# Kernel tuning notes

Hardware: AMD Instinct MI355X
Metric: run time of the kernel (lower is better)

Reference implementation:

```python
import jax, jax.numpy as jnp
import numpy as np
from jax.scipy.special import logsumexp

N, K, D = 131072, 256, 32


def setup_inputs() -> dict:
    key = jax.random.key(0)
    k1, k2, k3 = jax.random.split(key, 3)
    points = jax.random.normal(k1, (N, D), dtype=jnp.float32)
    centers = jax.random.uniform(k2, (K, D), dtype=jnp.float32)
    # well-conditioned inverse-sqrt covariances (original used 15*I; scaled to
    # avoid float32 overflow in sqrt(det(covs_inv)) for D=32)
    covs_inv_sqrt = (0.5 * jnp.broadcast_to(jnp.eye(D, dtype=jnp.float32), (K, D, D))
                     + 0.02 * jax.random.normal(k3, (K, D, D), dtype=jnp.float32))
    weights = jnp.ones((K,), dtype=jnp.float32)
    threshold = jnp.zeros((1,), dtype=jnp.float32)
    return {"points": points, "centers": centers,
            "covs_inv_sqrt": covs_inv_sqrt, "weights": weights,
            "threshold": threshold}


def reference(points, centers, covs_inv_sqrt, weights, threshold):
    # refresh(): equal_clusters=True branch
    w = jnp.abs(weights)
    center_prs = w / (w.sum() + 1e-30)                       # [K]
    covs_inv = jnp.einsum('kde,kfe->kdf', covs_inv_sqrt, covs_inv_sqrt)  # [K,D,D]
    coefs = center_prs * jnp.sqrt(jnp.linalg.det(covs_inv))  # [K]

    # pairwise weighted sqdist: q_ij = (x_i - c_j)^T A_j (x_i - c_j)
    B = covs_inv.reshape(K, D * D)                           # [K, D*D]
    X2 = (points[:, :, None] * points[:, None, :]).reshape(N, D * D)  # [N, D*D]
    t_xAx = X2 @ B.T                                         # [N, K]
    m = jnp.einsum('kde,ke->kd', covs_inv, centers)          # A_j c_j, [K,D]
    t_xAc = points @ m.T                                     # [N, K]
    t_cAc = jnp.einsum('kd,kd->k', m, centers)               # [K]
    d_ij = -0.5 * (t_xAx - 2.0 * t_xAc + t_cAc[None, :])     # [N, K]

    # weighted logsumexp over centers, then subtract threshold
    ll = logsumexp(d_ij, axis=1, b=coefs[None, :])           # [N]
    return ll[:, None] - threshold[0]                        # [N, 1]
```

## Files before the change

### kernel.cpp

```cpp
#include <hip/hip_runtime.h>
#include <math.h>

#define NPTS 131072
#define KCOMP 256
#define DIM 32
#define NREAL 560
#define NCH 18
#define PSIF_BYTES 294912
#define WS_NEED (PSIF_BYTES + KCOMP * 4)

typedef __attribute__((ext_vector_type(8))) short short8;
typedef __attribute__((ext_vector_type(16))) float f32x16;

__device__ __forceinline__ unsigned short f2bf(float v) {
    unsigned u = __float_as_uint(v);
    u += 0x7fffu + ((u >> 16) & 1u);
    return (unsigned short)(u >> 16);
}

__device__ __forceinline__ unsigned pkbf(float lo, float hi) {
#if __has_builtin(__builtin_amdgcn_perm)
    const unsigned a = __float_as_uint(hi) + 0x8000u;
    const unsigned b = __float_as_uint(lo) + 0x8000u;
    return __builtin_amdgcn_perm(a, b, 0x07060302u);
#else
    return (unsigned)f2bf(lo) | ((unsigned)f2bf(hi) << 16);
#endif
}

__device__ __forceinline__ void dma16(const uint4* g, uint4* s) {
    __builtin_amdgcn_global_load_lds(
        (const __attribute__((address_space(1))) void*)g,
        (__attribute__((address_space(3))) void*)s, 16, 0, 0);
}

constexpr int PfxT(int d) { return 32 * d - (d * (d - 1)) / 2; }
constexpr int rowT(int p) { int d = 0; while (d < 31 && PfxT(d + 1) <= p) ++d; return d; }
constexpr int colT(int p) { return rowT(p) + (p - PfxT(rowT(p))); }

template<int P, int J>
__device__ __forceinline__ float genOne(const float (&x)[DIM]) {
    constexpr int p = P + J;
    if constexpr (p >= NREAL) {
        return 0.f;
    } else if constexpr (p >= 528) {
        return x[p - 528];
    } else {
        constexpr int d = rowT(p);
        constexpr int f = colT(p);
        static_assert(d >= 0 && d < 32 && f >= d && f < 32, "bad feature map");
        return x[d] * x[f];
    }
}

__global__ __launch_bounds__(256) void gmm_pre(
    const float* __restrict__ S,
    const float* __restrict__ centers,
    const float* __restrict__ weights,
    unsigned short* __restrict__ PsiF,
    float* __restrict__ kc2)
{
    __shared__ float Sl[DIM][DIM + 1];
    __shared__ float As[DIM][DIM + 1];
    __shared__ float cl[DIM], ml[DIM];
    __shared__ float red[256];

    const int k = blockIdx.x, tid = threadIdx.x;

    for (int idx = tid; idx < DIM * DIM; idx += 256)
        Sl[idx >> 5][idx & 31] = S[(size_t)k * DIM * DIM + idx];
    if (tid < DIM) cl[tid] = centers[k * DIM + tid];
    __syncthreads();

    for (int idx = tid; idx < DIM * DIM; idx += 256) {
        const int d = idx >> 5, f = idx & 31;
        float a = 0.f;
#pragma unroll
        for (int e = 0; e < DIM; ++e) a = fmaf(Sl[d][e], Sl[f][e], a);
        As[d][f] = a;
    }
    __syncthreads();

    if (tid < DIM) {
        float mv = 0.f;
#pragma unroll
        for (int f = 0; f < DIM; ++f) mv = fmaf(As[tid][f], cl[f], mv);
        ml[tid] = mv;
    }
    __syncthreads();

    for (int p = tid; p < NREAL; p += 256) {
        float val;
        if (p < 528) {
            int d = 0, pr = 0;
            while (pr + (32 - d) <= p) { pr += (32 - d); ++d; }
            const int f = d + (p - pr);
            val = (f == d) ? -0.5f * As[d][d] : -As[d][f];
        } else {
            val = ml[p - 528];
        }
        const int c = p >> 6, kk = p & 63;
        const int s = kk >> 4, qq = (kk >> 3) & 1, j = kk & 7;
        const int ct = k >> 5, ll = qq * 32 + (k & 31);
        const int g = c * 2048 + (s * 8 + ct) * 64 + ll;
        PsiF[(size_t)g * 8 + j] = f2bf(val);
    }

    red[tid] = fabsf(weights[tid]);
    __syncthreads();
    for (int off = 128; off > 0; off >>= 1) {
        if (tid < off) red[tid] += red[tid + off];
        __syncthreads();
    }
    const float wsum = red[0];

    for (int j = 0; j < DIM - 1; ++j) {
        const float inv = 1.0f / As[j][j];
        for (int idx = tid; idx < DIM * DIM; idx += 256) {
            const int r = idx >> 5, c = idx & 31;
            if (r > j && c > j)
                As[r][c] = fmaf(-As[r][j] * inv, As[j][c], As[r][c]);
        }
        __syncthreads();
    }

    if (tid < DIM) red[tid] = __logf(As[tid][tid]);
    __syncthreads();
    if (tid == 0) {
        float sl = 0.f;
        for (int j = 0; j < DIM; ++j) sl += red[j];
        float cac = 0.f;
        for (int d2 = 0; d2 < DIM; ++d2) cac = fmaf(ml[d2], cl[d2], cac);
        kc2[k] = __logf(fabsf(weights[k])) - __logf(wsum + 1e-30f)
               + 0.5f * sl - 0.5f * cac;
    }
}

template<int P>
__device__ __forceinline__ void genQuad(const float (&x)[DIM], float* v) {
    v[0] = genOne<P, 0>(x);
    v[1] = genOne<P, 1>(x);
    v[2] = genOne<P, 2>(x);
    v[3] = genOne<P, 3>(x);
}

template<int CH, int SS>
__device__ __forceinline__ void genSite(const float (&x)[DIM], uint4* base,
                                        int rbg, int r32) {
    float v[8];
    genQuad<CH * 32 + SS * 8>(x, v);
    genQuad<CH * 32 + SS * 8 + 4>(x, v + 4);
    uint4 u;
    u.x = pkbf(v[0], v[1]);
    u.y = pkbf(v[2], v[3]);
    u.z = pkbf(v[4], v[5]);
    u.w = pkbf(v[6], v[7]);
    base[(SS >> 1) * 256 + rbg * 64 + (SS & 1) * 32 + r32] = u;
}

template<int CH>
__device__ __forceinline__ void genChunk(const float (&x)[DIM], uint4* sA4,
                                         int q, int rbg, int r32) {
    uint4* base = sA4 + (CH & 1) * 512;
    if constexpr (CH < 17) {
        if (q == 0)      genSite<CH, 0>(x, base, rbg, r32);
        else if (q == 1) genSite<CH, 1>(x, base, rbg, r32);
        else if (q == 2) genSite<CH, 2>(x, base, rbg, r32);
        else             genSite<CH, 3>(x, base, rbg, r32);
    } else {
        if (q == 0)      genSite<CH, 0>(x, base, rbg, r32);
        else if (q == 1) genSite<CH, 1>(x, base, rbg, r32);
    }
}

template<int C>
__device__ __forceinline__ void doChunk(const float (&x)[DIM],
    uint4* sA4, uint4* sB4, const uint4* __restrict__ PsiF4,
    f32x16 (&acc)[4],
    int l, int w, int q, int rbg, int r32, int rb, int c0)
{

    if constexpr (C + 1 < NCH) {
        constexpr int NI = (C + 1 == 17) ? 1 : 2;
        const uint4* src = PsiF4 + (C + 1) * 1024 + w * 64 + l;
        uint4* dst = sB4 + ((C + 1) & 1) * 1024 + w * 64 + l;
#pragma unroll
        for (int i = 0; i < NI; ++i) dma16(src + i * 512, dst + i * 512);
    }

    if constexpr (C + 1 < NCH) genChunk<C + 1>(x, sA4, q, rbg, r32);

    constexpr int NS = (C < 17) ? 2 : 1;
    const uint4* aa = sA4 + (C & 1) * 512;
    const uint4* bb = sB4 + (C & 1) * 1024;
#pragma unroll
    for (int s = 0; s < NS; ++s) {
        short8 a = __builtin_bit_cast(short8, aa[(s * 4 + rb) * 64 + l]);
#pragma unroll
        for (int j = 0; j < 4; ++j) {
            short8 b = __builtin_bit_cast(short8, bb[(s * 8 + c0 + j) * 64 + l]);
            acc[j] = __builtin_amdgcn_mfma_f32_32x32x16_bf16(a, b, acc[j], 0, 0, 0);
        }
    }

    __syncthreads();
}

__device__ __forceinline__ void epiHalf(const f32x16 (&acc)[4], const float (&kcv)[4],
    int rblock, int l, int whalf, float (*sM)[2], float (*sS)[2])
{
#pragma unroll
    for (int rg = 0; rg < 16; ++rg) {
        float vals[4], m = -INFINITY;
#pragma unroll
        for (int j = 0; j < 4; ++j) { vals[j] = acc[j][rg] + kcv[j]; m = fmaxf(m, vals[j]); }
#pragma unroll
        for (int mask = 1; mask < 32; mask <<= 1) m = fmaxf(m, __shfl_xor(m, mask, 64));
        float sv = 0.f;
#pragma unroll
        for (int j = 0; j < 4; ++j) sv += __expf(vals[j] - m);
#pragma unroll
        for (int mask = 1; mask < 32; mask <<= 1) sv += __shfl_xor(sv, mask, 64);
        if ((l & 31) == 0) {
            const int R = rblock * 32 + (rg & 3) + 8 * (rg >> 2) + 4 * (l >> 5);
            sM[R][whalf] = m; sS[R][whalf] = sv;
        }
    }
}

__global__ __launch_bounds__(512, 4) void gmm_mfma(
    const float* __restrict__ points,
    const unsigned short* __restrict__ PsiF,
    const float* __restrict__ kc2,
    const float* __restrict__ thr,
    float* __restrict__ out)
{
    __shared__ uint4 sA4[1024];
    __shared__ uint4 sB4[2048];
    float (*sM)[2] = (float (*)[2])sA4;
    float (*sS)[2] = (float (*)[2])(sA4 + 64);

    const int t = threadIdx.x;
    const int w = t >> 6, l = t & 63;
    const int row = t & 127, q = t >> 7;
    const int rbg = row >> 5, r32 = row & 31;
    const int rb = w >> 1, c0 = (w & 1) * 4;

    const uint4* PsiF4 = (const uint4*)PsiF;

    {
        const uint4* src = PsiF4 + w * 64 + l;
        uint4* dst = sB4 + w * 64 + l;
        dma16(src, dst);
        dma16(src + 512, dst + 512);
    }

    float x[DIM];
    const float4* px = (const float4*)(points + ((size_t)blockIdx.x * 128 + row) * DIM);
#pragma unroll
    for (int j2 = 0; j2 < 8; ++j2) {
        float4 v = px[j2];
        x[4 * j2 + 0] = v.x; x[4 * j2 + 1] = v.y;
        x[4 * j2 + 2] = v.z; x[4 * j2 + 3] = v.w;
    }

    f32x16 acc[4];
#pragma unroll
    for (int j = 0; j < 4; ++j)
#pragma unroll
        for (int r = 0; r < 16; ++r) acc[j][r] = 0.f;

    genChunk<0>(x, sA4, q, rbg, r32);
    __syncthreads();

    doChunk<0>(x, sA4, sB4, PsiF4, acc, l, w, q, rbg, r32, rb, c0);
    doChunk<1>(x, sA4, sB4, PsiF4, acc, l, w, q, rbg, r32, rb, c0);
    doChunk<2>(x, sA4, sB4, PsiF4, acc, l, w, q, rbg, r32, rb, c0);
    doChunk<3>(x, sA4, sB4, PsiF4, acc, l, w, q, rbg, r32, rb, c0);
    doChunk<4>(x, sA4, sB4, PsiF4, acc, l, w, q, rbg, r32, rb, c0);
    doChunk<5>(x, sA4, sB4, PsiF4, acc, l, w, q, rbg, r32, rb, c0);
    doChunk<6>(x, sA4, sB4, PsiF4, acc, l, w, q, rbg, r32, rb, c0);
    doChunk<7>(x, sA4, sB4, PsiF4, acc, l, w, q, rbg, r32, rb, c0);
    doChunk<8>(x, sA4, sB4, PsiF4, acc, l, w, q, rbg, r32, rb, c0);
    doChunk<9>(x, sA4, sB4, PsiF4, acc, l, w, q, rbg, r32, rb, c0);
    doChunk<10>(x, sA4, sB4, PsiF4, acc, l, w, q, rbg, r32, rb, c0);
    doChunk<11>(x, sA4, sB4, PsiF4, acc, l, w, q, rbg, r32, rb, c0);
    doChunk<12>(x, sA4, sB4, PsiF4, acc, l, w, q, rbg, r32, rb, c0);
    doChunk<13>(x, sA4, sB4, PsiF4, acc, l, w, q, rbg, r32, rb, c0);
    doChunk<14>(x, sA4, sB4, PsiF4, acc, l, w, q, rbg, r32, rb, c0);
    doChunk<15>(x, sA4, sB4, PsiF4, acc, l, w, q, rbg, r32, rb, c0);
    doChunk<16>(x, sA4, sB4, PsiF4, acc, l, w, q, rbg, r32, rb, c0);
    doChunk<17>(x, sA4, sB4, PsiF4, acc, l, w, q, rbg, r32, rb, c0);

    float kcv[4];
#pragma unroll
    for (int j = 0; j < 4; ++j) kcv[j] = kc2[(c0 + j) * 32 + (l & 31)];

    epiHalf(acc, kcv, rb, l, w & 1, sM, sS);
    __syncthreads();

    if (t < 128) {
        const float m0 = sM[t][0], m1 = sM[t][1];
        const float M = fmaxf(m0, m1);
        const float Sv = sS[t][0] * __expf(m0 - M) + sS[t][1] * __expf(m1 - M);
        out[(size_t)blockIdx.x * 128 + t] = M + __logf(Sv) - thr[0];
    }
}

extern "C" void kernel_launch(void* const* d_in, const int* in_sizes, int n_in,
                              void* d_out, int out_size, void* d_ws, size_t ws_size,
                              hipStream_t stream) {
    const float* points  = (const float*)d_in[0];
    const float* centers = (const float*)d_in[1];
    const float* covs    = (const float*)d_in[2];
    const float* weights = (const float*)d_in[3];
    const float* thr     = (const float*)d_in[4];
    float* out = (float*)d_out;

    unsigned short* PsiF = (unsigned short*)d_ws;
    float* kc2 = (float*)((char*)d_ws + PSIF_BYTES);

    gmm_pre<<<KCOMP, 256, 0, stream>>>(covs, centers, weights, PsiF, kc2);
    gmm_mfma<<<NPTS / 128, 512, 0, stream>>>(points, PsiF, kc2, thr, out);
}
```

Before: 139.3 us.

## Generate A fragments in registers, shrink block to 64 points, triple-buffer B

The points-side feature fragments are now built directly in registers for each MFMA instead of being staged through shared memory. The block tile shrinks to 64 points, with each wave covering 64 components instead of 128, and the grid doubles. The B tile now uses a three-stage ring with a prefetch distance of two, waited on with explicit vmcnt plus barrier. This removes the LDS write/read traffic for the A operand and one barrier per chunk, but every wave now recomputes the quadratic features (twice per k-step because of the half-wave select), and each B tile is reused across half as many points.

```diff
diff --git a/kernel.cpp b/kernel.cpp
--- a/kernel.cpp
+++ b/kernel.cpp
@@ -32,6 +32,16 @@
     __builtin_amdgcn_global_load_lds(
         (const __attribute__((address_space(1))) void*)g,
         (__attribute__((address_space(3))) void*)s, 16, 0, 0);
+}
+
+template<int N>
+__device__ __forceinline__ void waitbar() {
+    if constexpr (N == 2)
+        asm volatile("s_waitcnt vmcnt(2)\ns_barrier" ::: "memory");
+    else if constexpr (N == 1)
+        asm volatile("s_waitcnt vmcnt(1)\ns_barrier" ::: "memory");
+    else
+        asm volatile("s_waitcnt vmcnt(0)\ns_barrier" ::: "memory");
 }
 
 constexpr int PfxT(int d) { return 32 * d - (d * (d - 1)) / 2; }
@@ -136,96 +146,61 @@
     }
 }
 
-template<int P>
-__device__ __forceinline__ void genQuad(const float (&x)[DIM], float* v) {
-    v[0] = genOne<P, 0>(x);
-    v[1] = genOne<P, 1>(x);
-    v[2] = genOne<P, 2>(x);
-    v[3] = genOne<P, 3>(x);
-}
-
-template<int CH, int SS>
-__device__ __forceinline__ void genSite(const float (&x)[DIM], uint4* base,
-                                        int rbg, int r32) {
+template<int BASE>
+__device__ __forceinline__ uint4 packFrag(const float (&x)[DIM]) {
     float v[8];
-    genQuad<CH * 32 + SS * 8>(x, v);
-    genQuad<CH * 32 + SS * 8 + 4>(x, v + 4);
+    v[0] = genOne<BASE, 0>(x); v[1] = genOne<BASE, 1>(x);
+    v[2] = genOne<BASE, 2>(x); v[3] = genOne<BASE, 3>(x);
+    v[4] = genOne<BASE, 4>(x); v[5] = genOne<BASE, 5>(x);
+    v[6] = genOne<BASE, 6>(x); v[7] = genOne<BASE, 7>(x);
     uint4 u;
     u.x = pkbf(v[0], v[1]);
     u.y = pkbf(v[2], v[3]);
     u.z = pkbf(v[4], v[5]);
     u.w = pkbf(v[6], v[7]);
-    base[(SS >> 1) * 256 + rbg * 64 + (SS & 1) * 32 + r32] = u;
-}
-
-template<int CH>
-__device__ __forceinline__ void genChunk(const float (&x)[DIM], uint4* sA4,
-                                         int q, int rbg, int r32) {
-    uint4* base = sA4 + (CH & 1) * 512;
-    if constexpr (CH < 17) {
-        if (q == 0)      genSite<CH, 0>(x, base, rbg, r32);
-        else if (q == 1) genSite<CH, 1>(x, base, rbg, r32);
-        else if (q == 2) genSite<CH, 2>(x, base, rbg, r32);
-        else             genSite<CH, 3>(x, base, rbg, r32);
-    } else {
-        if (q == 0)      genSite<CH, 0>(x, base, rbg, r32);
-        else if (q == 1) genSite<CH, 1>(x, base, rbg, r32);
+    return u;
+}
+
+template<int C, int S>
+__device__ __forceinline__ void kstep(const float (&x)[DIM], const uint4* bb,
+                                      f32x16 (&acc)[2], int l, bool kgb, int cq)
+{
+    uint4 f0 = packFrag<C * 32 + S * 16 + 0>(x);
+    uint4 f1 = packFrag<C * 32 + S * 16 + 8>(x);
+    uint4 fs;
+    fs.x = kgb ? f1.x : f0.x;
+    fs.y = kgb ? f1.y : f0.y;
+    fs.z = kgb ? f1.z : f0.z;
+    fs.w = kgb ? f1.w : f0.w;
+    short8 a = __builtin_bit_cast(short8, fs);
+#pragma unroll
+    for (int j = 0; j < 2; ++j) {
+        short8 b = __builtin_bit_cast(short8, bb[(S * 8 + cq * 2 + j) * 64 + l]);
+        acc[j] = __builtin_amdgcn_mfma_f32_32x32x16_bf16(a, b, acc[j], 0, 0, 0);
     }
 }
 
 template<int C>
 __device__ __forceinline__ void doChunk(const float (&x)[DIM],
-    uint4* sA4, uint4* sB4, const uint4* __restrict__ PsiF4,
-    f32x16 (&acc)[4],
-    int l, int w, int q, int rbg, int r32, int rb, int c0)
+    uint4* sB4, const uint4* __restrict__ PsiF4, f32x16 (&acc)[2],
+    int l, int w, bool kgb, int cq)
 {
 
-    if constexpr (C + 1 < NCH) {
-        constexpr int NI = (C + 1 == 17) ? 1 : 2;
-        const uint4* src = PsiF4 + (C + 1) * 1024 + w * 64 + l;
-        uint4* dst = sB4 + ((C + 1) & 1) * 1024 + w * 64 + l;
+    if constexpr (C + 2 < NCH) {
+        constexpr int NI = (C + 2 == 17) ? 1 : 2;
+        const uint4* src = PsiF4 + (C + 2) * 1024 + w * 64 + l;
+        uint4* dst = sB4 + ((C + 2) % 3) * 1024 + w * 64 + l;
 #pragma unroll
         for (int i = 0; i < NI; ++i) dma16(src + i * 512, dst + i * 512);
     }
 
-    if constexpr (C + 1 < NCH) genChunk<C + 1>(x, sA4, q, rbg, r32);
-
-    constexpr int NS = (C < 17) ? 2 : 1;
-    const uint4* aa = sA4 + (C & 1) * 512;
-    const uint4* bb = sB4 + (C & 1) * 1024;
-#pragma unroll
-    for (int s = 0; s < NS; ++s) {
-        short8 a = __builtin_bit_cast(short8, aa[(s * 4 + rb) * 64 + l]);
-#pragma unroll
-        for (int j = 0; j < 4; ++j) {
-            short8 b = __builtin_bit_cast(short8, bb[(s * 8 + c0 + j) * 64 + l]);
-            acc[j] = __builtin_amdgcn_mfma_f32_32x32x16_bf16(a, b, acc[j], 0, 0, 0);
-        }
-    }
-
-    __syncthreads();
-}
-
-__device__ __forceinline__ void epiHalf(const f32x16 (&acc)[4], const float (&kcv)[4],
-    int rblock, int l, int whalf, float (*sM)[2], float (*sS)[2])
-{
-#pragma unroll
-    for (int rg = 0; rg < 16; ++rg) {
-        float vals[4], m = -INFINITY;
-#pragma unroll
-        for (int j = 0; j < 4; ++j) { vals[j] = acc[j][rg] + kcv[j]; m = fmaxf(m, vals[j]); }
-#pragma unroll
-        for (int mask = 1; mask < 32; mask <<= 1) m = fmaxf(m, __shfl_xor(m, mask, 64));
-        float sv = 0.f;
-#pragma unroll
-        for (int j = 0; j < 4; ++j) sv += __expf(vals[j] - m);
-#pragma unroll
-        for (int mask = 1; mask < 32; mask <<= 1) sv += __shfl_xor(sv, mask, 64);
-        if ((l & 31) == 0) {
-            const int R = rblock * 32 + (rg & 3) + 8 * (rg >> 2) + 4 * (l >> 5);
-            sM[R][whalf] = m; sS[R][whalf] = sv;
-        }
-    }
+    const uint4* bb = sB4 + (C % 3) * 1024;
+    kstep<C, 0>(x, bb, acc, l, kgb, cq);
+    if constexpr (C < 17) kstep<C, 1>(x, bb, acc, l, kgb, cq);
+
+    if constexpr (C <= 14)      waitbar<2>();
+    else if constexpr (C == 15) waitbar<1>();
+    else if constexpr (C == 16) waitbar<0>();
 }
 
 __global__ __launch_bounds__(512, 4) void gmm_mfma(
@@ -235,28 +210,29 @@
     const float* __restrict__ thr,
     float* __restrict__ out)
 {
-    __shared__ uint4 sA4[1024];
-    __shared__ uint4 sB4[2048];
-    float (*sM)[2] = (float (*)[2])sA4;
-    float (*sS)[2] = (float (*)[2])(sA4 + 64);
+    __shared__ uint4 sB4[3072];
+    float (*sM)[4] = (float (*)[4])sB4;
+    float (*sS)[4] = (float (*)[4])((float*)sB4 + 256);
 
     const int t = threadIdx.x;
     const int w = t >> 6, l = t & 63;
-    const int row = t & 127, q = t >> 7;
-    const int rbg = row >> 5, r32 = row & 31;
-    const int rb = w >> 1, c0 = (w & 1) * 4;
+    const bool kgb = (l >= 32);
+    const int rb2 = w >> 2, cq = w & 3;
+    const int row = rb2 * 32 + (l & 31);
 
     const uint4* PsiF4 = (const uint4*)PsiF;
 
     {
         const uint4* src = PsiF4 + w * 64 + l;
         uint4* dst = sB4 + w * 64 + l;
-        dma16(src, dst);
-        dma16(src + 512, dst + 512);
+        dma16(src,        dst);
+        dma16(src +  512, dst +  512);
+        dma16(src + 1024, dst + 1024);
+        dma16(src + 1536, dst + 1536);
     }
 
     float x[DIM];
-    const float4* px = (const float4*)(points + ((size_t)blockIdx.x * 128 + row) * DIM);
+    const float4* px = (const float4*)(points + ((size_t)blockIdx.x * 64 + row) * DIM);
 #pragma unroll
     for (int j2 = 0; j2 < 8; ++j2) {
         float4 v = px[j2];
@@ -264,46 +240,60 @@
         x[4 * j2 + 2] = v.z; x[4 * j2 + 3] = v.w;
     }
 
-    f32x16 acc[4];
-#pragma unroll
-    for (int j = 0; j < 4; ++j)
+    f32x16 acc[2];
+#pragma unroll
+    for (int j = 0; j < 2; ++j)
 #pragma unroll
         for (int r = 0; r < 16; ++r) acc[j][r] = 0.f;
 
-    genChunk<0>(x, sA4, q, rbg, r32);
-    __syncthreads();
-
-    doChunk<0>(x, sA4, sB4, PsiF4, acc, l, w, q, rbg, r32, rb, c0);
-    doChunk<1>(x, sA4, sB4, PsiF4, acc, l, w, q, rbg, r32, rb, c0);
-    doChunk<2>(x, sA4, sB4, PsiF4, acc, l, w, q, rbg, r32, rb, c0);
-    doChunk<3>(x, sA4, sB4, PsiF4, acc, l, w, q, rbg, r32, rb, c0);
-    doChunk<4>(x, sA4, sB4, PsiF4, acc, l, w, q, rbg, r32, rb, c0);
-    doChunk<5>(x, sA4, sB4, PsiF4, acc, l, w, q, rbg, r32, rb, c0);
-    doChunk<6>(x, sA4, sB4, PsiF4, acc, l, w, q, rbg, r32, rb, c0);
-    doChunk<7>(x, sA4, sB4, PsiF4, acc, l, w, q, rbg, r32, rb, c0);
-    doChunk<8>(x, sA4, sB4, PsiF4, acc, l, w, q, rbg, r32, rb, c0);
-    doChunk<9>(x, sA4, sB4, PsiF4, acc, l, w, q, rbg, r32, rb, c0);
-    doChunk<10>(x, sA4, sB4, PsiF4, acc, l, w, q, rbg, r32, rb, c0);
-    doChunk<11>(x, sA4, sB4, PsiF4, acc, l, w, q, rbg, r32, rb, c0);
-    doChunk<12>(x, sA4, sB4, PsiF4, acc, l, w, q, rbg, r32, rb, c0);
-    doChunk<13>(x, sA4, sB4, PsiF4, acc, l, w, q, rbg, r32, rb, c0);
-    doChunk<14>(x, sA4, sB4, PsiF4, acc, l, w, q, rbg, r32, rb, c0);
-    doChunk<15>(x, sA4, sB4, PsiF4, acc, l, w, q, rbg, r32, rb, c0);
-    doChunk<16>(x, sA4, sB4, PsiF4, acc, l, w, q, rbg, r32, rb, c0);
-    doChunk<17>(x, sA4, sB4, PsiF4, acc, l, w, q, rbg, r32, rb, c0);
-
-    float kcv[4];
-#pragma unroll
-    for (int j = 0; j < 4; ++j) kcv[j] = kc2[(c0 + j) * 32 + (l & 31)];
-
-    epiHalf(acc, kcv, rb, l, w & 1, sM, sS);
-    __syncthreads();
-
-    if (t < 128) {
-        const float m0 = sM[t][0], m1 = sM[t][1];
-        const float M = fmaxf(m0, m1);
-        const float Sv = sS[t][0] * __expf(m0 - M) + sS[t][1] * __expf(m1 - M);
-        out[(size_t)blockIdx.x * 128 + t] = M + __logf(Sv) - thr[0];
+    asm volatile("s_waitcnt vmcnt(0)\ns_barrier" ::: "memory");
+
+    doChunk<0>(x, sB4, PsiF4, acc, l, w, kgb, cq);
+    doChunk<1>(x, sB4, PsiF4, acc, l, w, kgb, cq);
+    doChunk<2>(x, sB4, PsiF4, acc, l, w, kgb, cq);
+    doChunk<3>(x, sB4, PsiF4, acc, l, w, kgb, cq);
+    doChunk<4>(x, sB4, PsiF4, acc, l, w, kgb, cq);
+    doChunk<5>(x, sB4, PsiF4, acc, l, w, kgb, cq);
+    doChunk<6>(x, sB4, PsiF4, acc, l, w, kgb, cq);
+    doChunk<7>(x, sB4, PsiF4, acc, l, w, kgb, cq);
+    doChunk<8>(x, sB4, PsiF4, acc, l, w, kgb, cq);
+    doChunk<9>(x, sB4, PsiF4, acc, l, w, kgb, cq);
+    doChunk<10>(x, sB4, PsiF4, acc, l, w, kgb, cq);
+    doChunk<11>(x, sB4, PsiF4, acc, l, w, kgb, cq);
+    doChunk<12>(x, sB4, PsiF4, acc, l, w, kgb, cq);
+    doChunk<13>(x, sB4, PsiF4, acc, l, w, kgb, cq);
+    doChunk<14>(x, sB4, PsiF4, acc, l, w, kgb, cq);
+    doChunk<15>(x, sB4, PsiF4, acc, l, w, kgb, cq);
+    doChunk<16>(x, sB4, PsiF4, acc, l, w, kgb, cq);
+    doChunk<17>(x, sB4, PsiF4, acc, l, w, kgb, cq);
+
+    float kcv[2];
+    kcv[0] = kc2[(cq * 2 + 0) * 32 + (l & 31)];
+    kcv[1] = kc2[(cq * 2 + 1) * 32 + (l & 31)];
+
+#pragma unroll
+    for (int rg = 0; rg < 16; ++rg) {
+        float v0 = acc[0][rg] + kcv[0];
+        float v1 = acc[1][rg] + kcv[1];
+        float m = fmaxf(v0, v1);
+#pragma unroll
+        for (int mask = 1; mask < 32; mask <<= 1) m = fmaxf(m, __shfl_xor(m, mask, 64));
+        float sv = __expf(v0 - m) + __expf(v1 - m);
+#pragma unroll
+        for (int mask = 1; mask < 32; mask <<= 1) sv += __shfl_xor(sv, mask, 64);
+        if ((l & 31) == 0) {
+            const int R = rb2 * 32 + (rg & 3) + 8 * (rg >> 2) + 4 * (l >> 5);
+            sM[R][cq] = m; sS[R][cq] = sv;
+        }
+    }
+    __syncthreads();
+
+    if (t < 64) {
+        const float m0 = sM[t][0], m1 = sM[t][1], m2 = sM[t][2], m3 = sM[t][3];
+        const float M = fmaxf(fmaxf(m0, m1), fmaxf(m2, m3));
+        const float Sv = sS[t][0] * __expf(m0 - M) + sS[t][1] * __expf(m1 - M)
+                       + sS[t][2] * __expf(m2 - M) + sS[t][3] * __expf(m3 - M);
+        out[(size_t)blockIdx.x * 64 + t] = M + __logf(Sv) - thr[0];
     }
 }
 
@@ -321,5 +311,5 @@
     float* kc2 = (float*)((char*)d_ws + PSIF_BYTES);
 
     gmm_pre<<<KCOMP, 256, 0, stream>>>(covs, centers, weights, PsiF, kc2);
-    gmm_mfma<<<NPTS / 128, 512, 0, stream>>>(points, PsiF, kc2, thr, out);
-}
+    gmm_mfma<<<NPTS / 64, 512, 0, stream>>>(points, PsiF, kc2, thr, out);
+}
```

Measured after the change: 180.0 us. 1.29x slower.
